# Optimization experiments

Measured on AMD Instinct MI355X. Metric: run time of the kernel, lower is better.

Reference implementation:

```python
import jax, jax.numpy as jnp
import numpy as np
from jax import lax

B, L, V = 128, 64, 8192
E = H = 128
STEPS = 10
MAX_BIN = 512
BETA_START, BETA_END = 1e-4, 2e-2


def setup_inputs():
    key = jax.random.key(0)
    k = jax.random.split(key, 23)
    s = 0.05
    padded_x = (jax.random.uniform(k[0], (B, L, V)) < 0.01).astype(jnp.float32)
    lengths = jax.random.randint(k[1], (B,), 1, L + 1)
    visit_mask = (jnp.arange(L)[None, :] < lengths[:, None]).astype(jnp.float32)
    padded_bins = jnp.sort(jax.random.randint(k[2], (B, L), 0, MAX_BIN), axis=1)
    t_diff = jax.random.randint(k[3], (B,), 1, STEPS + 1)
    eps = jax.random.normal(k[4], (B, L, E))
    z0 = jax.random.normal(k[5], (B, L, E))
    noise = jax.random.normal(k[6], (STEPS, B, L, E))
    W_visit = jax.random.normal(k[7], (E, V)) * s
    bin_embed = (jax.random.normal(k[8], (MAX_BIN + 2, E)) * s).at[0].set(0.0)  # padding_idx=0
    W_ih = jax.random.normal(k[9], (4 * H, E)) * s
    W_hh = jax.random.normal(k[10], (4 * H, H)) * s
    b_ih = jax.random.normal(k[11], (4 * H,)) * s
    b_hh = jax.random.normal(k[12], (4 * H,)) * s
    W_cls = jax.random.normal(k[13], (1, H)) * s
    b_cls = jax.random.normal(k[14], (1,)) * s
    W_proj = jax.random.normal(k[15], (E, H)) * s
    time_embed = jax.random.normal(k[16], (STEPS + 1, E)) * s
    W_fuse = jax.random.normal(k[17], (2, 2 * E)) * s
    b_fuse = jax.random.normal(k[18], (2,)) * s
    W_e1 = jax.random.normal(k[19], (E, 2 * E)) * s
    b_e1 = jax.random.normal(k[20], (E,)) * s
    W_e2 = jax.random.normal(k[21], (E, E)) * s
    b_e2 = jax.random.normal(k[22], (E,)) * s
    return dict(padded_x=padded_x, visit_mask=visit_mask, padded_bins=padded_bins,
                t_diff=t_diff, eps=eps, z0=z0, noise=noise, W_visit=W_visit,
                bin_embed=bin_embed, W_ih=W_ih, W_hh=W_hh, b_ih=b_ih, b_hh=b_hh,
                W_cls=W_cls, b_cls=b_cls, W_proj=W_proj, time_embed=time_embed,
                W_fuse=W_fuse, b_fuse=b_fuse, W_e1=W_e1, b_e1=b_e1, W_e2=W_e2, b_e2=b_e2)


def _lstm(v, W_ih, W_hh, b_ih, b_hh):
    # v: [B,L,E] -> h: [B,L,H]; PyTorch gate order i,f,g,o
    xg = jnp.einsum('ble,ge->blg', v, W_ih) + b_ih + b_hh
    def step(carry, x):
        h, c = carry
        g = x + h @ W_hh.T
        i, f, gg, o = jnp.split(g, 4, axis=-1)
        c = jax.nn.sigmoid(f) * c + jax.nn.sigmoid(i) * jnp.tanh(gg)
        h = jax.nn.sigmoid(o) * jnp.tanh(c)
        return (h, c), h
    z = jnp.zeros((v.shape[0], W_hh.shape[1]), v.dtype)
    _, hs = lax.scan(step, (z, z), jnp.swapaxes(xg, 0, 1))
    return jnp.swapaxes(hs, 0, 1)


def _last_hidden(h, mask):
    lengths = jnp.maximum(mask.sum(axis=1).astype(jnp.int32), 1)
    return h[jnp.arange(h.shape[0]), lengths - 1]


def reference(padded_x, visit_mask, padded_bins, t_diff, eps, z0, noise,
              W_visit, bin_embed, W_ih, W_hh, b_ih, b_hh, W_cls, b_cls,
              W_proj, time_embed, W_fuse, b_fuse, W_e1, b_e1, W_e2, b_e2):
    m = visit_mask[..., None]                      # [B,L,1]
    betas = jnp.linspace(BETA_START, BETA_END, STEPS)
    alphas = 1.0 - betas
    alpha_bars = jnp.cumprod(alphas)

    # visit embedding + time-gap (delta bin) embedding
    delta = jnp.concatenate([jnp.zeros_like(padded_bins[:, :1]),
                             jnp.clip(padded_bins[:, 1:] - padded_bins[:, :-1], 0)], axis=1)
    delta = jnp.where(visit_mask > 0, jnp.clip(delta, 0, MAX_BIN + 1), 0)
    v = (padded_x @ W_visit.T + bin_embed[delta]) * m  # [B,L,E]

    # encoder LSTM (packed seq == plain scan then zero padded suffix positions)
    h = _lstm(v, W_ih, W_hh, b_ih, b_hh) * m
    logits_real = (_last_hidden(h, visit_mask) @ W_cls.T + b_cls)[:, 0]

    h_prev = jnp.pad(h[:, :-1], ((0, 0), (1, 0), (0, 0)))
    hp = (h_prev @ W_proj.T) * m                   # [B,L,E]

    def fuse_eps(z, t_emb):
        a = jax.nn.softmax(jnp.concatenate([z, hp], -1) @ W_fuse.T + b_fuse, axis=-1)
        g = a[..., :1] * z + a[..., 1:] * hp
        x = jnp.concatenate([g, t_emb], -1)
        return jax.nn.relu(x @ W_e1.T + b_e1) @ W_e2.T + b_e2

    # diffusion loss
    t = jnp.where(visit_mask > 0, t_diff[:, None], 1)    # [B,L]
    ab = alpha_bars[t - 1][..., None]
    z_t = (jnp.sqrt(ab) * v + jnp.sqrt(1.0 - ab) * eps) * m
    eps_pred = fuse_eps(z_t, time_embed[t])
    denom = jnp.maximum(visit_mask.sum(), 1.0)
    diffusion_loss = jnp.sum((eps_pred - eps) ** 2 * m) / denom

    # reverse diffusion sampling of synthetic visit embeddings
    def step(z, inp):
        kk, nz = inp
        t_s = jnp.where(visit_mask > 0, kk, 1)
        e = fuse_eps(z, time_embed[t_s])
        beta = betas[kk - 1]
        mean = (z - beta / jnp.sqrt(1.0 - alpha_bars[kk - 1]) * e) / jnp.sqrt(alphas[kk - 1])
        z = jnp.where(kk > 1, mean + jnp.sqrt(beta) * nz, mean) * m
        return z, None

    ks = jnp.arange(STEPS, 0, -1)
    v_syn, _ = lax.scan(step, z0, (ks, noise))

    h_syn = _lstm(v_syn, W_ih, W_hh, b_ih, b_hh) * m
    logits_syn = (_last_hidden(h_syn, visit_mask) @ W_cls.T + b_cls)[:, 0]
    return logits_real, logits_syn, diffusion_loss
```

## Files before the change

### kernel.cpp

```cpp
#include <hip/hip_runtime.h>

#define B_ 128
#define L_ 64
#define V_ 8192
#define E_ 128
#define H_ 128
#define G4_ 512
#define NROW (B_*L_)
#define HSTRIDE 136
#define AS 136
#define XS 264
#define YS 136
#define ZS 132

typedef unsigned short u16;
typedef __attribute__((ext_vector_type(8))) short bf16x8;
typedef __attribute__((ext_vector_type(4))) float f32x4;

__device__ __forceinline__ float sigm(float x){ return 1.f/(1.f + __expf(-x)); }
__device__ __forceinline__ float ftanh(float x){ float e = __expf(2.f*x); return 1.f - 2.f/(e + 1.f); }
__device__ __forceinline__ u16 f2bf(float f){
    union { unsigned int i; float f; } x; x.f = f;
    unsigned int r = x.i + 0x7fff + ((x.i >> 16) & 1);
    return (u16)(r >> 16);
}
#define LBAR() asm volatile("s_waitcnt lgkmcnt(0)\ns_barrier" ::: "memory")

__device__ __forceinline__ bf16x8 pack8(const float* p){
    const float4* q = (const float4*)p;
    float4 a = q[0], b = q[1];
    bf16x8 f;
    f[0]=(short)f2bf(a.x); f[1]=(short)f2bf(a.y); f[2]=(short)f2bf(a.z); f[3]=(short)f2bf(a.w);
    f[4]=(short)f2bf(b.x); f[5]=(short)f2bf(b.y); f[6]=(short)f2bf(b.z); f[7]=(short)f2bf(b.w);
    return f;
}

__global__ __launch_bounds__(256) void k_transpose_wv(const float* __restrict__ Wv, float* __restrict__ WT){
    __shared__ float tile[16][129];
    int v0 = blockIdx.x * 16;
    int t = threadIdx.x;
    #pragma unroll
    for(int i=0;i<8;i++){
        int idx = i*256 + t; int e = idx >> 4; int vv = idx & 15;
        tile[vv][e] = Wv[(size_t)e*V_ + v0 + vv];
    }
    __syncthreads();
    #pragma unroll
    for(int i=0;i<8;i++){
        int idx = i*256 + t; int vv = idx >> 7; int e = idx & 127;
        WT[(size_t)(v0+vv)*E_ + e] = tile[vv][e];
    }
}

__global__ __launch_bounds__(256) void k_visit_embed(const float* __restrict__ px, const float* __restrict__ vmask,
                                                     const int* __restrict__ bins, const float* __restrict__ bemb,
                                                     const float* __restrict__ WT, float* __restrict__ v){
    __shared__ int idxs[512];
    __shared__ int cnt;
    __shared__ int dsh;
    __shared__ float msh;
    __shared__ float4 red[8][32];
    int row = blockIdx.x; int l = row & 63;
    int t = threadIdx.x;
    if(t==0){
        cnt = 0;
        float m = vmask[row];
        int d = 0;
        if(l > 0){ d = bins[row] - bins[row-1]; d = d < 0 ? 0 : (d > 513 ? 513 : d); }
        if(!(m > 0.f)) d = 0;
        dsh = d; msh = m;
    }
    __syncthreads();
    const uint4* xr4 = (const uint4*)(px + (size_t)row * V_);
    for(int i=t;i<2048;i+=256){
        uint4 u = xr4[i];
        unsigned int w[4] = {u.x,u.y,u.z,u.w};
        #pragma unroll
        for(int j=0;j<4;j++){
            if(w[j]){ int p = atomicAdd(&cnt,1); if(p<512) idxs[p] = i*4 + j; }
        }
    }
    __syncthreads();
    int n = cnt; if(n > 512) n = 512;
    int eq = t & 31, jg = t >> 5;
    float4 a4 = {0.f,0.f,0.f,0.f};
    for(int j=jg;j<n;j+=8){
        const float4* wr = (const float4*)(WT + (size_t)idxs[j]*E_);
        float4 wv = wr[eq];
        a4.x += wv.x; a4.y += wv.y; a4.z += wv.z; a4.w += wv.w;
    }
    red[jg][eq] = a4;
    __syncthreads();
    if(t < 32){
        float4 s = red[0][t];
        #pragma unroll
        for(int g=1;g<8;g++){
            float4 r = red[g][t];
            s.x += r.x; s.y += r.y; s.z += r.z; s.w += r.w;
        }
        const float4* bp = (const float4*)(bemb + dsh*E_);
        float4 bv = bp[t];
        float m = msh;
        float4 o;
        o.x = (s.x + bv.x)*m; o.y = (s.y + bv.y)*m; o.z = (s.z + bv.z)*m; o.w = (s.w + bv.w)*m;
        ((float4*)(v + (size_t)row*E_))[t] = o;
    }
}

__global__ __launch_bounds__(256,2) void k_gemm_xg(const float* __restrict__ A, const float* __restrict__ Wih,
                                                   const float* __restrict__ bih, const float* __restrict__ bhh,
                                                   float* __restrict__ xg){
    __shared__ __align__(16) u16 abuf[16*AS];
    int t = threadIdx.x, wave = t >> 6, lane = t & 63, quad = lane >> 4, lc = lane & 15;
    int row0 = blockIdx.x * 16;
    #pragma unroll
    for(int i=0;i<8;i++){
        int flat = i*256 + t; int r = flat >> 7, e = flat & 127;
        abuf[r*AS + e] = f2bf(A[(size_t)(row0+r)*E_ + e]);
    }
    bf16x8 wfr[8][4]; float bb[8];
    #pragma unroll
    for(int nt=0;nt<8;nt++){
        int n = wave*128 + nt*16 + lc;
        bb[nt] = bih[n] + bhh[n];
        const float* wr = Wih + (size_t)n*E_ + quad*8;
        #pragma unroll
        for(int kt=0;kt<4;kt++) wfr[nt][kt] = pack8(wr + kt*32);
    }
    __syncthreads();
    f32x4 acc[8];
    #pragma unroll
    for(int nt=0;nt<8;nt++) acc[nt] = (f32x4){0.f,0.f,0.f,0.f};
    #pragma unroll
    for(int kt=0;kt<4;kt++){
        bf16x8 af = *(const bf16x8*)&abuf[lc*AS + kt*32 + quad*8];
        #pragma unroll
        for(int nt=0;nt<8;nt++)
            acc[nt] = __builtin_amdgcn_mfma_f32_16x16x32_bf16(af, wfr[nt][kt], acc[nt], 0,0,0);
    }
    #pragma unroll
    for(int nt=0;nt<8;nt++){
        int n = wave*128 + nt*16 + lc;
        #pragma unroll
        for(int r=0;r<4;r++)
            xg[(size_t)(row0 + quad*4 + r)*G4_ + n] = acc[nt][r] + bb[nt];
    }
}

__device__ __forceinline__ void lstm_step(int l, const float* pxg, float* ph,
        const u16* bufr, u16* bufw, const bf16x8 (&bf)[4][4],
        float (&xcur)[4][4], float (&xnxt)[4][4], float (&c4)[4],
        const float* vmsh, int lc, int quad, int wave, bool pf){
    bf16x8 af[4];
    #pragma unroll
    for(int kt=0;kt<4;kt++)
        af[kt] = *(const bf16x8*)&bufr[lc*HSTRIDE + kt*32 + quad*8];
    if(pf){
        #pragma unroll
        for(int gate=0;gate<4;gate++){
            #pragma unroll
            for(int r=0;r<4;r++)
                xnxt[gate][r] = pxg[(size_t)r*64*G4_ + (size_t)(l+1)*G4_ + gate*128];
        }
    }
    f32x4 acc[4];
    #pragma unroll
    for(int a=0;a<4;a++) acc[a] = (f32x4){0.f,0.f,0.f,0.f};
    #pragma unroll
    for(int kt=0;kt<4;kt++){
        #pragma unroll
        for(int a=0;a<4;a++)
            acc[a] = __builtin_amdgcn_mfma_f32_16x16x32_bf16(af[kt], bf[a][kt], acc[a], 0,0,0);
    }
    #pragma unroll
    for(int r=0;r<4;r++){
        float m = vmsh[(quad*4+r)*64 + l];
        float gi = acc[0][r] + xcur[0][r];
        float gf = acc[1][r] + xcur[1][r];
        float gg = acc[2][r] + xcur[2][r];
        float go = acc[3][r] + xcur[3][r];
        float c  = sigm(gf)*c4[r] + sigm(gi)*ftanh(gg);
        float h  = sigm(go)*ftanh(c);
        c4[r] = c;
        bufw[(quad*4+r)*HSTRIDE + wave*16 + lc] = f2bf(h);
        ph[(size_t)r*64*H_ + (size_t)l*H_] = h * m;
    }
    LBAR();
}

__global__ __launch_bounds__(512,2) void k_lstm_mfma(const float* __restrict__ xg, const float* __restrict__ Whh,
                                                     const float* __restrict__ vmask, float* __restrict__ hout){
    __shared__ u16 hbuf[2][16*HSTRIDE];
    __shared__ float vmsh[16*64];
    int t = threadIdx.x;
    int wave = t >> 6, lane = t & 63;
    int quad = lane >> 4, lc = lane & 15;
    int b0 = blockIdx.x * 16;

    for(int i=t;i<16*HSTRIDE;i+=512) hbuf[0][i] = 0;
    for(int i=t;i<1024;i+=512) vmsh[i] = vmask[b0*64 + i];

    bf16x8 bf[4][4];
    #pragma unroll
    for(int gate=0;gate<4;gate++){
        int n = gate*128 + wave*16 + lc;
        const float* wr = Whh + (size_t)n*H_ + quad*8;
        #pragma unroll
        for(int kt=0;kt<4;kt++) bf[gate][kt] = pack8(wr + kt*32);
    }

    float c4[4] = {0.f,0.f,0.f,0.f};

    const float* pxg = xg + ((size_t)(b0 + quad*4))*64*G4_ + wave*16 + lc;
    float* ph = hout + ((size_t)(b0 + quad*4))*64*H_ + wave*16 + lc;

    float xgv0[4][4], xgv1[4][4];
    #pragma unroll
    for(int gate=0;gate<4;gate++){
        #pragma unroll
        for(int r=0;r<4;r++)
            xgv0[gate][r] = pxg[(size_t)r*64*G4_ + gate*128];
    }
    __syncthreads();

    for(int lb=0;lb<64;lb+=2){
        lstm_step(lb,   pxg, ph, hbuf[0], hbuf[1], bf, xgv0, xgv1, c4, vmsh, lc, quad, wave, true);
        lstm_step(lb+1, pxg, ph, hbuf[1], hbuf[0], bf, xgv1, xgv0, c4, vmsh, lc, quad, wave, (lb+1) < 63);
    }
}

__global__ __launch_bounds__(256,2) void k_hp(const float* __restrict__ h, const float* __restrict__ Wproj,
                                              const float* __restrict__ vmask, float* __restrict__ hp){
    __shared__ __align__(16) u16 abuf[16*AS];
    int t = threadIdx.x, wave = t >> 6, lane = t & 63, quad = lane >> 4, lc = lane & 15;
    int row0 = blockIdx.x * 16;
    #pragma unroll
    for(int i=0;i<8;i++){
        int flat = i*256 + t; int r = flat >> 7, e = flat & 127;
        int row = row0 + r;
        float hv = (row & 63) ? h[(size_t)(row-1)*H_ + e] : 0.f;
        abuf[r*AS + e] = f2bf(hv);
    }
    bf16x8 wfr[2][4];
    #pragma unroll
    for(int nt=0;nt<2;nt++){
        int n = wave*32 + nt*16 + lc;
        const float* wr = Wproj + (size_t)n*H_ + quad*8;
        #pragma unroll
        for(int kt=0;kt<4;kt++) wfr[nt][kt] = pack8(wr + kt*32);
    }
    __syncthreads();
    f32x4 acc[2];
    acc[0] = (f32x4){0.f,0.f,0.f,0.f}; acc[1] = (f32x4){0.f,0.f,0.f,0.f};
    #pragma unroll
    for(int kt=0;kt<4;kt++){
        bf16x8 af = *(const bf16x8*)&abuf[lc*AS + kt*32 + quad*8];
        acc[0] = __builtin_amdgcn_mfma_f32_16x16x32_bf16(af, wfr[0][kt], acc[0], 0,0,0);
        acc[1] = __builtin_amdgcn_mfma_f32_16x16x32_bf16(af, wfr[1][kt], acc[1], 0,0,0);
    }
    #pragma unroll
    for(int nt=0;nt<2;nt++){
        int n = wave*32 + nt*16 + lc;
        #pragma unroll
        for(int r=0;r<4;r++){
            int row = row0 + quad*4 + r;
            hp[(size_t)row*E_ + n] = acc[nt][r] * vmask[row];
        }
    }
}

__global__ void k_logits(const float* __restrict__ h, const float* __restrict__ vmask,
                         const float* __restrict__ Wcls, const float* __restrict__ bcls, float* __restrict__ out){
    int b = blockIdx.x; int t = threadIdx.x;
    float s = vmask[b*64 + t];
    #pragma unroll
    for(int off=32;off;off>>=1) s += __shfl_down(s, off);
    s = __shfl(s, 0);
    int len = (int)(s + 0.5f); if(len < 1) len = 1;
    const float* hr = h + (size_t)(b*64 + len - 1)*H_;
    float val = hr[t]*Wcls[t] + hr[t+64]*Wcls[t+64];
    #pragma unroll
    for(int off=32;off;off>>=1) val += __shfl_down(val, off);
    if(t==0) out[b] = val + bcls[0];
}

__global__ __launch_bounds__(256,2) void k_diff_loss_mfma(const float* __restrict__ v, const float* __restrict__ hp,
        const float* __restrict__ eps, const int* __restrict__ tdiff, const float* __restrict__ vmask,
        const float* __restrict__ temb, const float* __restrict__ Wf, const float* __restrict__ bfu,
        const float* __restrict__ We1, const float* __restrict__ be1,
        const float* __restrict__ We2, const float* __restrict__ be2, float* __restrict__ partial){
    __shared__ float zbuf[16*ZS], hpbuf[16*ZS];
    __shared__ __align__(16) u16 xbuf[16*XS];
    __shared__ __align__(16) u16 y1buf[16*YS];
    __shared__ float wfsh[512];
    __shared__ float ssh[16][2], hpd[16][2];
    __shared__ float mrow[16]; __shared__ int trow[16];
    __shared__ float sabar[10];
    __shared__ float rb[4];
    int row0 = blockIdx.x * 16; int t = threadIdx.x;
    int wave = t >> 6, lane = t & 63, quad = lane >> 4, lc = lane & 15;

    if(t==0){
        float p = 1.f;
        for(int k=0;k<10;k++){ float b = 1e-4f + (0.02f - 1e-4f)*k/9.f; p *= (1.f - b); sabar[k] = p; }
    }
    if(t < 16){
        int row = row0 + t; float m = vmask[row];
        mrow[t] = m; trow[t] = (m > 0.f) ? tdiff[row >> 6] : 1;
    }
    for(int i=t;i<512;i+=256) wfsh[i] = Wf[i];
    __syncthreads();
    #pragma unroll
    for(int i=0;i<8;i++){
        int flat = i*256 + t; int r = flat >> 7; int e = flat & 127; int row = row0 + r;
        float ab = sabar[trow[r]-1];
        zbuf[r*ZS + e] = (sqrtf(ab)*v[(size_t)row*E_ + e] + sqrtf(1.f - ab)*eps[(size_t)row*E_ + e]) * mrow[r];
        hpbuf[r*ZS + e] = hp[(size_t)row*E_ + e];
    }
    bf16x8 wf1[2][8], wf2[2][4];
    float be1v[2], be2v[2];
    #pragma unroll
    for(int nt=0;nt<2;nt++){
        int n = wave*32 + nt*16 + lc;
        be1v[nt] = be1[n]; be2v[nt] = be2[n];
        const float* w1 = We1 + (size_t)n*256 + quad*8;
        #pragma unroll
        for(int kt=0;kt<8;kt++) wf1[nt][kt] = pack8(w1 + kt*32);
        const float* w2 = We2 + (size_t)n*128 + quad*8;
        #pragma unroll
        for(int kt=0;kt<4;kt++) wf2[nt][kt] = pack8(w2 + kt*32);
    }
    __syncthreads();
    {
        int row = t >> 4, k = (t >> 3) & 1, sub = t & 7;
        float p = 0.f, q = 0.f;
        #pragma unroll
        for(int i=0;i<16;i++){
            p += hpbuf[row*ZS + sub*16 + i] * wfsh[k*256 + 128 + sub*16 + i];
            q += zbuf[row*ZS + sub*16 + i]  * wfsh[k*256 + sub*16 + i];
        }
        p += __shfl_down(p,4); p += __shfl_down(p,2); p += __shfl_down(p,1);
        q += __shfl_down(q,4); q += __shfl_down(q,2); q += __shfl_down(q,1);
        if(sub == 0){ hpd[row][k] = p + bfu[k]; ssh[row][k] = q; }
    }
    __syncthreads();
    {
        int row = t >> 4, c0 = (t & 15) * 16;
        float s0 = ssh[row][0] + hpd[row][0], s1 = ssh[row][1] + hpd[row][1];
        float a0 = 1.f/(1.f + __expf(s1 - s0)), a1 = 1.f - a0;
        int tt = trow[row];
        #pragma unroll
        for(int i=0;i<16;i++){
            int c = c0 + i;
            float val = (c < 128) ? (a0*zbuf[row*ZS + c] + a1*hpbuf[row*ZS + c])
                                  : temb[tt*E_ + (c - 128)];
            xbuf[row*XS + c] = f2bf(val);
        }
    }
    __syncthreads();
    f32x4 acc1[2];
    acc1[0] = (f32x4){0.f,0.f,0.f,0.f}; acc1[1] = (f32x4){0.f,0.f,0.f,0.f};
    #pragma unroll
    for(int kt=0;kt<8;kt++){
        bf16x8 af = *(const bf16x8*)&xbuf[lc*XS + kt*32 + quad*8];
        acc1[0] = __builtin_amdgcn_mfma_f32_16x16x32_bf16(af, wf1[0][kt], acc1[0], 0,0,0);
        acc1[1] = __builtin_amdgcn_mfma_f32_16x16x32_bf16(af, wf1[1][kt], acc1[1], 0,0,0);
    }
    #pragma unroll
    for(int nt=0;nt<2;nt++){
        #pragma unroll
        for(int r=0;r<4;r++)
            y1buf[(quad*4+r)*YS + wave*32 + nt*16 + lc] = f2bf(fmaxf(acc1[nt][r] + be1v[nt], 0.f));
    }
    __syncthreads();
    f32x4 acc2[2];
    acc2[0] = (f32x4){0.f,0.f,0.f,0.f}; acc2[1] = (f32x4){0.f,0.f,0.f,0.f};
    #pragma unroll
    for(int kt=0;kt<4;kt++){
        bf16x8 af = *(const bf16x8*)&y1buf[lc*YS + kt*32 + quad*8];
        acc2[0] = __builtin_amdgcn_mfma_f32_16x16x32_bf16(af, wf2[0][kt], acc2[0], 0,0,0);
        acc2[1] = __builtin_amdgcn_mfma_f32_16x16x32_bf16(af, wf2[1][kt], acc2[1], 0,0,0);
    }
    float lp = 0.f;
    #pragma unroll
    for(int nt=0;nt<2;nt++){
        int n = wave*32 + nt*16 + lc;
        #pragma unroll
        for(int r=0;r<4;r++){
            int m = quad*4 + r;
            float d = (acc2[nt][r] + be2v[nt]) - eps[(size_t)(row0+m)*E_ + n];
            lp += d*d*mrow[m];
        }
    }
    #pragma unroll
    for(int off=32;off;off>>=1) lp += __shfl_down(lp, off);
    if(lane == 0) rb[wave] = lp;
    __syncthreads();
    if(t == 0) partial[blockIdx.x] = rb[0]+rb[1]+rb[2]+rb[3];
}

__global__ __launch_bounds__(256,2) void k_reverse_mfma(const float* __restrict__ hp, const float* __restrict__ z0,
        const float* __restrict__ noise, const float* __restrict__ vmask, const float* __restrict__ temb,
        const float* __restrict__ Wf, const float* __restrict__ bfu,
        const float* __restrict__ We1, const float* __restrict__ be1,
        const float* __restrict__ We2, const float* __restrict__ be2, float* __restrict__ vsyn){
    __shared__ float zbuf[16*ZS], hpbuf[16*ZS];
    __shared__ __align__(16) u16 xbuf[16*XS];
    __shared__ __align__(16) u16 y1buf[16*YS];
    __shared__ float wfsh[512];
    __shared__ float ssh[16][2], hpd[16][2];
    __shared__ float mrow[16];
    __shared__ float sbeta[10], sabar[10];
    int row0 = blockIdx.x * 16; int t = threadIdx.x;
    int wave = t >> 6, lane = t & 63, quad = lane >> 4, lc = lane & 15;

    if(t==0){
        float p = 1.f;
        for(int k=0;k<10;k++){ float b = 1e-4f + (0.02f - 1e-4f)*k/9.f; sbeta[k] = b; p *= (1.f - b); sabar[k] = p; }
    }
    if(t < 16) mrow[t] = vmask[row0 + t];
    for(int i=t;i<512;i+=256) wfsh[i] = Wf[i];
    #pragma unroll
    for(int i=0;i<8;i++){
        int flat = i*256 + t; int r = flat >> 7; int e = flat & 127; int row = row0 + r;
        zbuf[r*ZS + e]  = z0[(size_t)row*E_ + e];
        hpbuf[r*ZS + e] = hp[(size_t)row*E_ + e];
    }
    bf16x8 wf1[2][8], wf2[2][4];
    float be1v[2], be2v[2];
    #pragma unroll
    for(int nt=0;nt<2;nt++){
        int n = wave*32 + nt*16 + lc;
        be1v[nt] = be1[n]; be2v[nt] = be2[n];
        const float* w1 = We1 + (size_t)n*256 + quad*8;
        #pragma unroll
        for(int kt=0;kt<8;kt++) wf1[nt][kt] = pack8(w1 + kt*32);
        const float* w2 = We2 + (size_t)n*128 + quad*8;
        #pragma unroll
        for(int kt=0;kt<4;kt++) wf2[nt][kt] = pack8(w2 + kt*32);
    }
    __syncthreads();
    {
        int row = t >> 4, k = (t >> 3) & 1, sub = t & 7;
        float p = 0.f;
        #pragma unroll
        for(int i=0;i<16;i++)
            p += hpbuf[row*ZS + sub*16 + i] * wfsh[k*256 + 128 + sub*16 + i];
        p += __shfl_down(p,4); p += __shfl_down(p,2); p += __shfl_down(p,1);
        if(sub == 0) hpd[row][k] = p + bfu[k];
    }
    __syncthreads();

    for(int s=0;s<10;s++){
        int kk = 10 - s;
        {
            int row = t >> 4, k = (t >> 3) & 1, sub = t & 7;
            float q = 0.f;
            #pragma unroll
            for(int i=0;i<16;i++)
                q += zbuf[row*ZS + sub*16 + i] * wfsh[k*256 + sub*16 + i];
            q += __shfl_down(q,4); q += __shfl_down(q,2); q += __shfl_down(q,1);
            if(sub == 0) ssh[row][k] = q + hpd[row][k];
        }
        __syncthreads();
        {
            int row = t >> 4, c0 = (t & 15) * 16;
            float s0 = ssh[row][0], s1 = ssh[row][1];
            float a0 = 1.f/(1.f + __expf(s1 - s0)), a1 = 1.f - a0;
            int tt = (mrow[row] > 0.f) ? kk : 1;
            #pragma unroll
            for(int i=0;i<16;i++){
                int c = c0 + i;
                float val = (c < 128) ? (a0*zbuf[row*ZS + c] + a1*hpbuf[row*ZS + c])
                                      : temb[tt*E_ + (c - 128)];
                xbuf[row*XS + c] = f2bf(val);
            }
        }
        __syncthreads();
        f32x4 acc1[2];
        acc1[0] = (f32x4){0.f,0.f,0.f,0.f}; acc1[1] = (f32x4){0.f,0.f,0.f,0.f};
        #pragma unroll
        for(int kt=0;kt<8;kt++){
            bf16x8 af = *(const bf16x8*)&xbuf[lc*XS + kt*32 + quad*8];
            acc1[0] = __builtin_amdgcn_mfma_f32_16x16x32_bf16(af, wf1[0][kt], acc1[0], 0,0,0);
            acc1[1] = __builtin_amdgcn_mfma_f32_16x16x32_bf16(af, wf1[1][kt], acc1[1], 0,0,0);
        }
        #pragma unroll
        for(int nt=0;nt<2;nt++){
            #pragma unroll
            for(int r=0;r<4;r++)
                y1buf[(quad*4+r)*YS + wave*32 + nt*16 + lc] = f2bf(fmaxf(acc1[nt][r] + be1v[nt], 0.f));
        }
        __syncthreads();
        f32x4 acc2[2];
        acc2[0] = (f32x4){0.f,0.f,0.f,0.f}; acc2[1] = (f32x4){0.f,0.f,0.f,0.f};
        #pragma unroll
        for(int kt=0;kt<4;kt++){
            bf16x8 af = *(const bf16x8*)&y1buf[lc*YS + kt*32 + quad*8];
            acc2[0] = __builtin_amdgcn_mfma_f32_16x16x32_bf16(af, wf2[0][kt], acc2[0], 0,0,0);
            acc2[1] = __builtin_amdgcn_mfma_f32_16x16x32_bf16(af, wf2[1][kt], acc2[1], 0,0,0);
        }
        float beta = sbeta[kk-1];
        float c1 = beta / sqrtf(1.f - sabar[kk-1]);
        float c2 = 1.f / sqrtf(1.f - beta);
        float sb = sqrtf(beta);
        #pragma unroll
        for(int nt=0;nt<2;nt++){
            int n = wave*32 + nt*16 + lc;
            #pragma unroll
            for(int r=0;r<4;r++){
                int m = quad*4 + r;
                float e = acc2[nt][r] + be2v[nt];
                float z = zbuf[m*ZS + n];
                float mean = (z - c1*e) * c2;
                float nz = noise[((size_t)s*NROW + row0 + m)*E_ + n];
                float znew = (kk > 1) ? (mean + sb*nz) : mean;
                zbuf[m*ZS + n] = znew * mrow[m];
            }
        }
        __syncthreads();
    }
    {
        int row = t >> 4, c0 = (t & 15) * 16;
        if(c0 < 128){
            #pragma unroll
            for(int i=0;i<16;i++)
                vsyn[(size_t)(row0+row)*E_ + c0 + i] = zbuf[row*ZS + c0 + i];
        }
    }
}

__global__ void k_finalize(const float* __restrict__ partial, const float* __restrict__ vmask, float* __restrict__ out){
    __shared__ float rb[4], rl[4];
    int t = threadIdx.x;
    float s = 0.f;
    for(int i=t;i<NROW;i+=256) s += vmask[i];
    float ls = 0.f;
    for(int i=t;i<512;i+=256) ls += partial[i];
    #pragma unroll
    for(int off=32;off;off>>=1){ s += __shfl_down(s, off); ls += __shfl_down(ls, off); }
    if((t & 63) == 0){ rb[t >> 6] = s; rl[t >> 6] = ls; }
    __syncthreads();
    if(t == 0){
        float denom = rb[0]+rb[1]+rb[2]+rb[3];
        if(denom < 1.f) denom = 1.f;
        out[256] = (rl[0]+rl[1]+rl[2]+rl[3]) / denom;
    }
}

extern "C" void kernel_launch(void* const* d_in, const int* in_sizes, int n_in,
                              void* d_out, int out_size, void* d_ws, size_t ws_size,
                              hipStream_t stream){
    const float* px    = (const float*)d_in[0];
    const float* vmask = (const float*)d_in[1];
    const int*   bins  = (const int*)d_in[2];
    const int*   tdiff = (const int*)d_in[3];
    const float* eps   = (const float*)d_in[4];
    const float* z0    = (const float*)d_in[5];
    const float* noise = (const float*)d_in[6];
    const float* Wv    = (const float*)d_in[7];
    const float* bemb  = (const float*)d_in[8];
    const float* Wih   = (const float*)d_in[9];
    const float* Whh   = (const float*)d_in[10];
    const float* bih   = (const float*)d_in[11];
    const float* bhh   = (const float*)d_in[12];
    const float* Wcls  = (const float*)d_in[13];
    const float* bcls  = (const float*)d_in[14];
    const float* Wproj = (const float*)d_in[15];
    const float* temb  = (const float*)d_in[16];
    const float* Wf    = (const float*)d_in[17];
    const float* bfu   = (const float*)d_in[18];
    const float* We1   = (const float*)d_in[19];
    const float* be1   = (const float*)d_in[20];
    const float* We2   = (const float*)d_in[21];
    const float* be2   = (const float*)d_in[22];
    float* out = (float*)d_out;

    float* ws      = (float*)d_ws;
    float* WT      = ws;
    float* v       = ws + 1048576;
    float* xg      = ws + 2097152;
    float* h       = ws + 6291456;
    float* hp      = ws + 7340032;
    float* vsyn    = ws + 8388608;
    float* partial = ws + 9437184;

    hipLaunchKernelGGL(k_transpose_wv, dim3(V_/16), dim3(256), 0, stream, Wv, WT);
    hipLaunchKernelGGL(k_visit_embed, dim3(NROW), dim3(256), 0, stream, px, vmask, bins, bemb, WT, v);
    hipLaunchKernelGGL(k_gemm_xg, dim3(NROW/16), dim3(256), 0, stream, v, Wih, bih, bhh, xg);
    hipLaunchKernelGGL(k_lstm_mfma, dim3(B_/16), dim3(512), 0, stream, xg, Whh, vmask, h);
    hipLaunchKernelGGL(k_logits, dim3(B_), dim3(64), 0, stream, h, vmask, Wcls, bcls, out);
    hipLaunchKernelGGL(k_hp, dim3(NROW/16), dim3(256), 0, stream, h, Wproj, vmask, hp);
    hipLaunchKernelGGL(k_diff_loss_mfma, dim3(NROW/16), dim3(256), 0, stream,
                       v, hp, eps, tdiff, vmask, temb, Wf, bfu, We1, be1, We2, be2, partial);
    hipLaunchKernelGGL(k_reverse_mfma, dim3(NROW/16), dim3(256), 0, stream,
                       hp, z0, noise, vmask, temb, Wf, bfu, We1, be1, We2, be2, vsyn);
    hipLaunchKernelGGL(k_gemm_xg, dim3(NROW/16), dim3(256), 0, stream, vsyn, Wih, bih, bhh, xg);
    hipLaunchKernelGGL(k_lstm_mfma, dim3(B_/16), dim3(512), 0, stream, xg, Whh, vmask, h);
    hipLaunchKernelGGL(k_logits, dim3(B_), dim3(64), 0, stream, h, vmask, Wcls, bcls, out + 128);
    hipLaunchKernelGGL(k_finalize, dim3(1), dim3(256), 0, stream, partial, vmask, out);
}
```

Measured before the change: 828.7 us.

## Fuse LSTM with projection and logits; merge diffusion loss, reverse sampling and input GEMM

Folds the hp projection (h_{t-1} @ Wproj) into the LSTM recurrence as an extra MFMA per step, and computes the classifier logit inside the LSTM, so the h tensor is no longer materialized. The diffusion-loss pass runs as step zero of the reverse-sampling kernel, and the second input-gate GEMM runs at the end of that same kernel. This removes several launches and round trips of h, hp and v_syn through global memory. In exchange the serial LSTM loop carries extra MFMA work and stores per step, and the fused diffusion kernel holds more weights in registers, which may lower occupancy.

```diff
diff --git a/kernel.cpp b/kernel.cpp
--- a/kernel.cpp
+++ b/kernel.cpp
@@ -147,34 +147,44 @@
     }
 }
 
-__device__ __forceinline__ void lstm_step(int l, const float* pxg, float* ph,
-        const u16* bufr, u16* bufw, const bf16x8 (&bf)[4][4],
-        float (&xcur)[4][4], float (&xnxt)[4][4], float (&c4)[4],
-        const float* vmsh, int lc, int quad, int wave, bool pf){
+__device__ __forceinline__ void lstm_step(int l, const float* pxg, float* hp_out, bool dohp,
+        const u16* bufr, u16* bufw, const bf16x8 (&bf)[4][4], const bf16x8 (&wp)[4],
+        float (&xcur)[4][4], float (&xnxt)[4][4], float (&c4)[4], float (&lg4)[4],
+        const int (&len4)[4], float wcv,
+        const float* vmsh, int lc, int quad, int wave, int b0){
+    if(l+1 < 64){
+        #pragma unroll
+        for(int gate=0;gate<4;gate++){
+            #pragma unroll
+            for(int r=0;r<4;r++)
+                xnxt[gate][r] = pxg[(size_t)r*64*G4_ + (size_t)(l+1)*G4_ + gate*128];
+        }
+    }
     bf16x8 af[4];
     #pragma unroll
     for(int kt=0;kt<4;kt++)
         af[kt] = *(const bf16x8*)&bufr[lc*HSTRIDE + kt*32 + quad*8];
-    if(pf){
-        #pragma unroll
-        for(int gate=0;gate<4;gate++){
-            #pragma unroll
-            for(int r=0;r<4;r++)
-                xnxt[gate][r] = pxg[(size_t)r*64*G4_ + (size_t)(l+1)*G4_ + gate*128];
-        }
-    }
-    f32x4 acc[4];
+    f32x4 acc[4], acch;
     #pragma unroll
     for(int a=0;a<4;a++) acc[a] = (f32x4){0.f,0.f,0.f,0.f};
+    acch = (f32x4){0.f,0.f,0.f,0.f};
     #pragma unroll
     for(int kt=0;kt<4;kt++){
         #pragma unroll
         for(int a=0;a<4;a++)
             acc[a] = __builtin_amdgcn_mfma_f32_16x16x32_bf16(af[kt], bf[a][kt], acc[a], 0,0,0);
+        acch = __builtin_amdgcn_mfma_f32_16x16x32_bf16(af[kt], wp[kt], acch, 0,0,0);
+    }
+    if(dohp){
+        #pragma unroll
+        for(int r=0;r<4;r++){
+            float m = vmsh[(quad*4+r)*64 + l];
+            int grow = (b0 + quad*4 + r)*64 + l;
+            hp_out[(size_t)grow*E_ + wave*16 + lc] = acch[r] * m;
+        }
     }
     #pragma unroll
     for(int r=0;r<4;r++){
-        float m = vmsh[(quad*4+r)*64 + l];
         float gi = acc[0][r] + xcur[0][r];
         float gf = acc[1][r] + xcur[1][r];
         float gg = acc[2][r] + xcur[2][r];
@@ -183,36 +193,55 @@
         float h  = sigm(go)*ftanh(c);
         c4[r] = c;
         bufw[(quad*4+r)*HSTRIDE + wave*16 + lc] = f2bf(h);
-        ph[(size_t)r*64*H_ + (size_t)l*H_] = h * m;
+        if(l == len4[r]-1) lg4[r] += h * wcv;
     }
     LBAR();
 }
 
-__global__ __launch_bounds__(512,2) void k_lstm_mfma(const float* __restrict__ xg, const float* __restrict__ Whh,
-                                                     const float* __restrict__ vmask, float* __restrict__ hout){
+__global__ __launch_bounds__(512,2) void k_lstm_fused(const float* __restrict__ xg, const float* __restrict__ Whh,
+        const float* __restrict__ Wproj, const float* __restrict__ Wcls, const float* __restrict__ bcls,
+        const float* __restrict__ vmask, float* __restrict__ hp_out, float* __restrict__ logits_out){
     __shared__ u16 hbuf[2][16*HSTRIDE];
     __shared__ float vmsh[16*64];
+    __shared__ int lensh[16];
+    __shared__ float lgsh[16][132];
     int t = threadIdx.x;
     int wave = t >> 6, lane = t & 63;
     int quad = lane >> 4, lc = lane & 15;
     int b0 = blockIdx.x * 16;
+    bool dohp = (hp_out != nullptr);
 
     for(int i=t;i<16*HSTRIDE;i+=512) hbuf[0][i] = 0;
     for(int i=t;i<1024;i+=512) vmsh[i] = vmask[b0*64 + i];
-
+    __syncthreads();
+    if(t < 16){
+        int s = 0;
+        #pragma unroll
+        for(int i=0;i<64;i++) s += (vmsh[t*64 + i] > 0.f) ? 1 : 0;
+        lensh[t] = s < 1 ? 1 : s;
+    }
+
+    int cw = wave*16 + lc;
     bf16x8 bf[4][4];
     #pragma unroll
     for(int gate=0;gate<4;gate++){
-        int n = gate*128 + wave*16 + lc;
+        int n = gate*128 + cw;
         const float* wr = Whh + (size_t)n*H_ + quad*8;
         #pragma unroll
         for(int kt=0;kt<4;kt++) bf[gate][kt] = pack8(wr + kt*32);
     }
+    bf16x8 wp[4];
+    {
+        const float* wr = Wproj + (size_t)cw*H_ + quad*8;
+        #pragma unroll
+        for(int kt=0;kt<4;kt++) wp[kt] = pack8(wr + kt*32);
+    }
+    float wcv = Wcls[cw];
 
     float c4[4] = {0.f,0.f,0.f,0.f};
-
-    const float* pxg = xg + ((size_t)(b0 + quad*4))*64*G4_ + wave*16 + lc;
-    float* ph = hout + ((size_t)(b0 + quad*4))*64*H_ + wave*16 + lc;
+    float lg4[4] = {0.f,0.f,0.f,0.f};
+
+    const float* pxg = xg + ((size_t)(b0 + quad*4))*64*G4_ + cw;
 
     float xgv0[4][4], xgv1[4][4];
     #pragma unroll
@@ -222,87 +251,51 @@
             xgv0[gate][r] = pxg[(size_t)r*64*G4_ + gate*128];
     }
     __syncthreads();
+    int len4[4];
+    #pragma unroll
+    for(int r=0;r<4;r++) len4[r] = lensh[quad*4 + r];
 
     for(int lb=0;lb<64;lb+=2){
-        lstm_step(lb,   pxg, ph, hbuf[0], hbuf[1], bf, xgv0, xgv1, c4, vmsh, lc, quad, wave, true);
-        lstm_step(lb+1, pxg, ph, hbuf[1], hbuf[0], bf, xgv1, xgv0, c4, vmsh, lc, quad, wave, (lb+1) < 63);
-    }
-}
-
-__global__ __launch_bounds__(256,2) void k_hp(const float* __restrict__ h, const float* __restrict__ Wproj,
-                                              const float* __restrict__ vmask, float* __restrict__ hp){
-    __shared__ __align__(16) u16 abuf[16*AS];
-    int t = threadIdx.x, wave = t >> 6, lane = t & 63, quad = lane >> 4, lc = lane & 15;
-    int row0 = blockIdx.x * 16;
-    #pragma unroll
-    for(int i=0;i<8;i++){
-        int flat = i*256 + t; int r = flat >> 7, e = flat & 127;
-        int row = row0 + r;
-        float hv = (row & 63) ? h[(size_t)(row-1)*H_ + e] : 0.f;
-        abuf[r*AS + e] = f2bf(hv);
-    }
-    bf16x8 wfr[2][4];
-    #pragma unroll
-    for(int nt=0;nt<2;nt++){
-        int n = wave*32 + nt*16 + lc;
-        const float* wr = Wproj + (size_t)n*H_ + quad*8;
-        #pragma unroll
-        for(int kt=0;kt<4;kt++) wfr[nt][kt] = pack8(wr + kt*32);
-    }
-    __syncthreads();
-    f32x4 acc[2];
-    acc[0] = (f32x4){0.f,0.f,0.f,0.f}; acc[1] = (f32x4){0.f,0.f,0.f,0.f};
-    #pragma unroll
-    for(int kt=0;kt<4;kt++){
-        bf16x8 af = *(const bf16x8*)&abuf[lc*AS + kt*32 + quad*8];
-        acc[0] = __builtin_amdgcn_mfma_f32_16x16x32_bf16(af, wfr[0][kt], acc[0], 0,0,0);
-        acc[1] = __builtin_amdgcn_mfma_f32_16x16x32_bf16(af, wfr[1][kt], acc[1], 0,0,0);
-    }
-    #pragma unroll
-    for(int nt=0;nt<2;nt++){
-        int n = wave*32 + nt*16 + lc;
-        #pragma unroll
-        for(int r=0;r<4;r++){
-            int row = row0 + quad*4 + r;
-            hp[(size_t)row*E_ + n] = acc[nt][r] * vmask[row];
-        }
-    }
-}
-
-__global__ void k_logits(const float* __restrict__ h, const float* __restrict__ vmask,
-                         const float* __restrict__ Wcls, const float* __restrict__ bcls, float* __restrict__ out){
-    int b = blockIdx.x; int t = threadIdx.x;
-    float s = vmask[b*64 + t];
-    #pragma unroll
-    for(int off=32;off;off>>=1) s += __shfl_down(s, off);
-    s = __shfl(s, 0);
-    int len = (int)(s + 0.5f); if(len < 1) len = 1;
-    const float* hr = h + (size_t)(b*64 + len - 1)*H_;
-    float val = hr[t]*Wcls[t] + hr[t+64]*Wcls[t+64];
-    #pragma unroll
-    for(int off=32;off;off>>=1) val += __shfl_down(val, off);
-    if(t==0) out[b] = val + bcls[0];
-}
-
-__global__ __launch_bounds__(256,2) void k_diff_loss_mfma(const float* __restrict__ v, const float* __restrict__ hp,
+        lstm_step(lb,   pxg, hp_out, dohp, hbuf[0], hbuf[1], bf, wp, xgv0, xgv1, c4, lg4, len4, wcv, vmsh, lc, quad, wave, b0);
+        lstm_step(lb+1, pxg, hp_out, dohp, hbuf[1], hbuf[0], bf, wp, xgv1, xgv0, c4, lg4, len4, wcv, vmsh, lc, quad, wave, b0);
+    }
+    #pragma unroll
+    for(int r=0;r<4;r++) lgsh[quad*4+r][cw] = lg4[r];
+    __syncthreads();
+    {
+        int row = t >> 5, l32 = t & 31;
+        float s = lgsh[row][l32] + lgsh[row][l32+32] + lgsh[row][l32+64] + lgsh[row][l32+96];
+        s += __shfl_down(s, 16, 32);
+        s += __shfl_down(s, 8, 32);
+        s += __shfl_down(s, 4, 32);
+        s += __shfl_down(s, 2, 32);
+        s += __shfl_down(s, 1, 32);
+        if(l32 == 0) logits_out[b0 + row] = s + bcls[0];
+    }
+}
+
+__global__ __launch_bounds__(256,2) void k_drg(const float* __restrict__ v, const float* __restrict__ hp,
         const float* __restrict__ eps, const int* __restrict__ tdiff, const float* __restrict__ vmask,
-        const float* __restrict__ temb, const float* __restrict__ Wf, const float* __restrict__ bfu,
+        const float* __restrict__ z0, const float* __restrict__ noise, const float* __restrict__ temb,
+        const float* __restrict__ Wf, const float* __restrict__ bfu,
         const float* __restrict__ We1, const float* __restrict__ be1,
-        const float* __restrict__ We2, const float* __restrict__ be2, float* __restrict__ partial){
+        const float* __restrict__ We2, const float* __restrict__ be2,
+        const float* __restrict__ Wih, const float* __restrict__ bih, const float* __restrict__ bhh,
+        float* __restrict__ partial, float* __restrict__ xg2){
     __shared__ float zbuf[16*ZS], hpbuf[16*ZS];
     __shared__ __align__(16) u16 xbuf[16*XS];
     __shared__ __align__(16) u16 y1buf[16*YS];
     __shared__ float wfsh[512];
     __shared__ float ssh[16][2], hpd[16][2];
     __shared__ float mrow[16]; __shared__ int trow[16];
-    __shared__ float sabar[10];
+    __shared__ float sbeta[10], sabar[10];
     __shared__ float rb[4];
     int row0 = blockIdx.x * 16; int t = threadIdx.x;
     int wave = t >> 6, lane = t & 63, quad = lane >> 4, lc = lane & 15;
 
     if(t==0){
         float p = 1.f;
-        for(int k=0;k<10;k++){ float b = 1e-4f + (0.02f - 1e-4f)*k/9.f; p *= (1.f - b); sabar[k] = p; }
+        for(int k=0;k<10;k++){ float b = 1e-4f + (0.02f - 1e-4f)*k/9.f; sbeta[k] = b; p *= (1.f - b); sabar[k] = p; }
     }
     if(t < 16){
         int row = row0 + t; float m = vmask[row];
@@ -333,115 +326,6 @@
     __syncthreads();
     {
         int row = t >> 4, k = (t >> 3) & 1, sub = t & 7;
-        float p = 0.f, q = 0.f;
-        #pragma unroll
-        for(int i=0;i<16;i++){
-            p += hpbuf[row*ZS + sub*16 + i] * wfsh[k*256 + 128 + sub*16 + i];
-            q += zbuf[row*ZS + sub*16 + i]  * wfsh[k*256 + sub*16 + i];
-        }
-        p += __shfl_down(p,4); p += __shfl_down(p,2); p += __shfl_down(p,1);
-        q += __shfl_down(q,4); q += __shfl_down(q,2); q += __shfl_down(q,1);
-        if(sub == 0){ hpd[row][k] = p + bfu[k]; ssh[row][k] = q; }
-    }
-    __syncthreads();
-    {
-        int row = t >> 4, c0 = (t & 15) * 16;
-        float s0 = ssh[row][0] + hpd[row][0], s1 = ssh[row][1] + hpd[row][1];
-        float a0 = 1.f/(1.f + __expf(s1 - s0)), a1 = 1.f - a0;
-        int tt = trow[row];
-        #pragma unroll
-        for(int i=0;i<16;i++){
-            int c = c0 + i;
-            float val = (c < 128) ? (a0*zbuf[row*ZS + c] + a1*hpbuf[row*ZS + c])
-                                  : temb[tt*E_ + (c - 128)];
-            xbuf[row*XS + c] = f2bf(val);
-        }
-    }
-    __syncthreads();
-    f32x4 acc1[2];
-    acc1[0] = (f32x4){0.f,0.f,0.f,0.f}; acc1[1] = (f32x4){0.f,0.f,0.f,0.f};
-    #pragma unroll
-    for(int kt=0;kt<8;kt++){
-        bf16x8 af = *(const bf16x8*)&xbuf[lc*XS + kt*32 + quad*8];
-        acc1[0] = __builtin_amdgcn_mfma_f32_16x16x32_bf16(af, wf1[0][kt], acc1[0], 0,0,0);
-        acc1[1] = __builtin_amdgcn_mfma_f32_16x16x32_bf16(af, wf1[1][kt], acc1[1], 0,0,0);
-    }
-    #pragma unroll
-    for(int nt=0;nt<2;nt++){
-        #pragma unroll
-        for(int r=0;r<4;r++)
-            y1buf[(quad*4+r)*YS + wave*32 + nt*16 + lc] = f2bf(fmaxf(acc1[nt][r] + be1v[nt], 0.f));
-    }
-    __syncthreads();
-    f32x4 acc2[2];
-    acc2[0] = (f32x4){0.f,0.f,0.f,0.f}; acc2[1] = (f32x4){0.f,0.f,0.f,0.f};
-    #pragma unroll
-    for(int kt=0;kt<4;kt++){
-        bf16x8 af = *(const bf16x8*)&y1buf[lc*YS + kt*32 + quad*8];
-        acc2[0] = __builtin_amdgcn_mfma_f32_16x16x32_bf16(af, wf2[0][kt], acc2[0], 0,0,0);
-        acc2[1] = __builtin_amdgcn_mfma_f32_16x16x32_bf16(af, wf2[1][kt], acc2[1], 0,0,0);
-    }
-    float lp = 0.f;
-    #pragma unroll
-    for(int nt=0;nt<2;nt++){
-        int n = wave*32 + nt*16 + lc;
-        #pragma unroll
-        for(int r=0;r<4;r++){
-            int m = quad*4 + r;
-            float d = (acc2[nt][r] + be2v[nt]) - eps[(size_t)(row0+m)*E_ + n];
-            lp += d*d*mrow[m];
-        }
-    }
-    #pragma unroll
-    for(int off=32;off;off>>=1) lp += __shfl_down(lp, off);
-    if(lane == 0) rb[wave] = lp;
-    __syncthreads();
-    if(t == 0) partial[blockIdx.x] = rb[0]+rb[1]+rb[2]+rb[3];
-}
-
-__global__ __launch_bounds__(256,2) void k_reverse_mfma(const float* __restrict__ hp, const float* __restrict__ z0,
-        const float* __restrict__ noise, const float* __restrict__ vmask, const float* __restrict__ temb,
-        const float* __restrict__ Wf, const float* __restrict__ bfu,
-        const float* __restrict__ We1, const float* __restrict__ be1,
-        const float* __restrict__ We2, const float* __restrict__ be2, float* __restrict__ vsyn){
-    __shared__ float zbuf[16*ZS], hpbuf[16*ZS];
-    __shared__ __align__(16) u16 xbuf[16*XS];
-    __shared__ __align__(16) u16 y1buf[16*YS];
-    __shared__ float wfsh[512];
-    __shared__ float ssh[16][2], hpd[16][2];
-    __shared__ float mrow[16];
-    __shared__ float sbeta[10], sabar[10];
-    int row0 = blockIdx.x * 16; int t = threadIdx.x;
-    int wave = t >> 6, lane = t & 63, quad = lane >> 4, lc = lane & 15;
-
-    if(t==0){
-        float p = 1.f;
-        for(int k=0;k<10;k++){ float b = 1e-4f + (0.02f - 1e-4f)*k/9.f; sbeta[k] = b; p *= (1.f - b); sabar[k] = p; }
-    }
-    if(t < 16) mrow[t] = vmask[row0 + t];
-    for(int i=t;i<512;i+=256) wfsh[i] = Wf[i];
-    #pragma unroll
-    for(int i=0;i<8;i++){
-        int flat = i*256 + t; int r = flat >> 7; int e = flat & 127; int row = row0 + r;
-        zbuf[r*ZS + e]  = z0[(size_t)row*E_ + e];
-        hpbuf[r*ZS + e] = hp[(size_t)row*E_ + e];
-    }
-    bf16x8 wf1[2][8], wf2[2][4];
-    float be1v[2], be2v[2];
-    #pragma unroll
-    for(int nt=0;nt<2;nt++){
-        int n = wave*32 + nt*16 + lc;
-        be1v[nt] = be1[n]; be2v[nt] = be2[n];
-        const float* w1 = We1 + (size_t)n*256 + quad*8;
-        #pragma unroll
-        for(int kt=0;kt<8;kt++) wf1[nt][kt] = pack8(w1 + kt*32);
-        const float* w2 = We2 + (size_t)n*128 + quad*8;
-        #pragma unroll
-        for(int kt=0;kt<4;kt++) wf2[nt][kt] = pack8(w2 + kt*32);
-    }
-    __syncthreads();
-    {
-        int row = t >> 4, k = (t >> 3) & 1, sub = t & 7;
         float p = 0.f;
         #pragma unroll
         for(int i=0;i<16;i++)
@@ -451,8 +335,8 @@
     }
     __syncthreads();
 
-    for(int s=0;s<10;s++){
-        int kk = 10 - s;
+    for(int s=0;s<11;s++){
+        int kk = 10 - (s - 1);
         {
             int row = t >> 4, k = (t >> 3) & 1, sub = t & 7;
             float q = 0.f;
@@ -467,7 +351,7 @@
             int row = t >> 4, c0 = (t & 15) * 16;
             float s0 = ssh[row][0], s1 = ssh[row][1];
             float a0 = 1.f/(1.f + __expf(s1 - s0)), a1 = 1.f - a0;
-            int tt = (mrow[row] > 0.f) ? kk : 1;
+            int tt = (s == 0) ? trow[row] : ((mrow[row] > 0.f) ? kk : 1);
             #pragma unroll
             for(int i=0;i<16;i++){
                 int c = c0 + i;
@@ -500,33 +384,83 @@
             acc2[0] = __builtin_amdgcn_mfma_f32_16x16x32_bf16(af, wf2[0][kt], acc2[0], 0,0,0);
             acc2[1] = __builtin_amdgcn_mfma_f32_16x16x32_bf16(af, wf2[1][kt], acc2[1], 0,0,0);
         }
-        float beta = sbeta[kk-1];
-        float c1 = beta / sqrtf(1.f - sabar[kk-1]);
-        float c2 = 1.f / sqrtf(1.f - beta);
-        float sb = sqrtf(beta);
-        #pragma unroll
-        for(int nt=0;nt<2;nt++){
-            int n = wave*32 + nt*16 + lc;
-            #pragma unroll
-            for(int r=0;r<4;r++){
-                int m = quad*4 + r;
-                float e = acc2[nt][r] + be2v[nt];
-                float z = zbuf[m*ZS + n];
-                float mean = (z - c1*e) * c2;
-                float nz = noise[((size_t)s*NROW + row0 + m)*E_ + n];
-                float znew = (kk > 1) ? (mean + sb*nz) : mean;
-                zbuf[m*ZS + n] = znew * mrow[m];
+        if(s == 0){
+            float lp = 0.f;
+            #pragma unroll
+            for(int nt=0;nt<2;nt++){
+                int n = wave*32 + nt*16 + lc;
+                #pragma unroll
+                for(int r=0;r<4;r++){
+                    int m = quad*4 + r;
+                    float d = (acc2[nt][r] + be2v[nt]) - eps[(size_t)(row0+m)*E_ + n];
+                    lp += d*d*mrow[m];
+                }
             }
-        }
-        __syncthreads();
+            #pragma unroll
+            for(int off=32;off;off>>=1) lp += __shfl_down(lp, off);
+            if(lane == 0) rb[wave] = lp;
+            __syncthreads();
+            if(t == 0) partial[blockIdx.x] = rb[0]+rb[1]+rb[2]+rb[3];
+            #pragma unroll
+            for(int i=0;i<8;i++){
+                int flat = i*256 + t; int r = flat >> 7; int e = flat & 127;
+                zbuf[r*ZS + e] = z0[(size_t)(row0+r)*E_ + e];
+            }
+            __syncthreads();
+        } else {
+            float beta = sbeta[kk-1];
+            float c1 = beta / sqrtf(1.f - sabar[kk-1]);
+            float c2 = 1.f / sqrtf(1.f - beta);
+            float sb = sqrtf(beta);
+            #pragma unroll
+            for(int nt=0;nt<2;nt++){
+                int n = wave*32 + nt*16 + lc;
+                #pragma unroll
+                for(int r=0;r<4;r++){
+                    int m = quad*4 + r;
+                    float e = acc2[nt][r] + be2v[nt];
+                    float z = zbuf[m*ZS + n];
+                    float mean = (z - c1*e) * c2;
+                    float nz = noise[((size_t)(s-1)*NROW + row0 + m)*E_ + n];
+                    float znew = (kk > 1) ? (mean + sb*nz) : mean;
+                    zbuf[m*ZS + n] = znew * mrow[m];
+                }
+            }
+            __syncthreads();
+        }
     }
     {
-        int row = t >> 4, c0 = (t & 15) * 16;
-        if(c0 < 128){
-            #pragma unroll
-            for(int i=0;i<16;i++)
-                vsyn[(size_t)(row0+row)*E_ + c0 + i] = zbuf[row*ZS + c0 + i];
-        }
+        int row = t >> 4, c0 = (t & 15) * 8;
+        #pragma unroll
+        for(int i=0;i<8;i++)
+            xbuf[row*XS + c0 + i] = f2bf(zbuf[row*ZS + c0 + i]);
+    }
+    __syncthreads();
+    bf16x8 wg[8][4]; float bb[8];
+    #pragma unroll
+    for(int nt=0;nt<8;nt++){
+        int n = wave*128 + nt*16 + lc;
+        bb[nt] = bih[n] + bhh[n];
+        const float* wr = Wih + (size_t)n*E_ + quad*8;
+        #pragma unroll
+        for(int kt=0;kt<4;kt++) wg[nt][kt] = pack8(wr + kt*32);
+    }
+    f32x4 ac[8];
+    #pragma unroll
+    for(int nt=0;nt<8;nt++) ac[nt] = (f32x4){0.f,0.f,0.f,0.f};
+    #pragma unroll
+    for(int kt=0;kt<4;kt++){
+        bf16x8 af = *(const bf16x8*)&xbuf[lc*XS + kt*32 + quad*8];
+        #pragma unroll
+        for(int nt=0;nt<8;nt++)
+            ac[nt] = __builtin_amdgcn_mfma_f32_16x16x32_bf16(af, wg[nt][kt], ac[nt], 0,0,0);
+    }
+    #pragma unroll
+    for(int nt=0;nt<8;nt++){
+        int n = wave*128 + nt*16 + lc;
+        #pragma unroll
+        for(int r=0;r<4;r++)
+            xg2[(size_t)(row0 + quad*4 + r)*G4_ + n] = ac[nt][r] + bb[nt];
     }
 }
 
@@ -580,23 +514,18 @@
     float* WT      = ws;
     float* v       = ws + 1048576;
     float* xg      = ws + 2097152;
-    float* h       = ws + 6291456;
-    float* hp      = ws + 7340032;
-    float* vsyn    = ws + 8388608;
-    float* partial = ws + 9437184;
+    float* hp      = ws + 6291456;
+    float* partial = ws + 7340032;
 
     hipLaunchKernelGGL(k_transpose_wv, dim3(V_/16), dim3(256), 0, stream, Wv, WT);
     hipLaunchKernelGGL(k_visit_embed, dim3(NROW), dim3(256), 0, stream, px, vmask, bins, bemb, WT, v);
     hipLaunchKernelGGL(k_gemm_xg, dim3(NROW/16), dim3(256), 0, stream, v, Wih, bih, bhh, xg);
-    hipLaunchKernelGGL(k_lstm_mfma, dim3(B_/16), dim3(512), 0, stream, xg, Whh, vmask, h);
-    hipLaunchKernelGGL(k_logits, dim3(B_), dim3(64), 0, stream, h, vmask, Wcls, bcls, out);
-    hipLaunchKernelGGL(k_hp, dim3(NROW/16), dim3(256), 0, stream, h, Wproj, vmask, hp);
-    hipLaunchKernelGGL(k_diff_loss_mfma, dim3(NROW/16), dim3(256), 0, stream,
-                       v, hp, eps, tdiff, vmask, temb, Wf, bfu, We1, be1, We2, be2, partial);
-    hipLaunchKernelGGL(k_reverse_mfma, dim3(NROW/16), dim3(256), 0, stream,
-                       hp, z0, noise, vmask, temb, Wf, bfu, We1, be1, We2, be2, vsyn);
-    hipLaunchKernelGGL(k_gemm_xg, dim3(NROW/16), dim3(256), 0, stream, vsyn, Wih, bih, bhh, xg);
-    hipLaunchKernelGGL(k_lstm_mfma, dim3(B_/16), dim3(512), 0, stream, xg, Whh, vmask, h);
-    hipLaunchKernelGGL(k_logits, dim3(B_), dim3(64), 0, stream, h, vmask, Wcls, bcls, out + 128);
+    hipLaunchKernelGGL(k_lstm_fused, dim3(B_/16), dim3(512), 0, stream,
+                       xg, Whh, Wproj, Wcls, bcls, vmask, hp, out);
+    hipLaunchKernelGGL(k_drg, dim3(NROW/16), dim3(256), 0, stream,
+                       v, hp, eps, tdiff, vmask, z0, noise, temb, Wf, bfu,
+                       We1, be1, We2, be2, Wih, bih, bhh, partial, xg);
+    hipLaunchKernelGGL(k_lstm_fused, dim3(B_/16), dim3(512), 0, stream,
+                       xg, Whh, Wproj, Wcls, bcls, vmask, (float*)nullptr, out + 128);
     hipLaunchKernelGGL(k_finalize, dim3(1), dim3(256), 0, stream, partial, vmask, out);
 }
```

Result: no change. 816.7 us, median of 2 (-1.4%).
